# Kernel optimization log

Measured on AMD Instinct MI355X. Metric: run time of the kernel, lower is better.

## Reference

```python
import jax, jax.numpy as jnp
import numpy as np

B, S, D, H, Dh, F = 1, 2048, 2048, 24, 128, 8192  # batch, seq, dim, heads, dim_head, ff hidden
SCALE = Dh ** -0.5


def _layernorm(x, g, b, eps=1e-5):
    mu = jnp.mean(x, axis=-1, keepdims=True)
    var = jnp.var(x, axis=-1, keepdims=True)
    return (x - mu) * jax.lax.rsqrt(var + eps) * g + b


def _rmsnorm(x, g, eps=1e-5):
    ms = jnp.mean(jnp.square(x), axis=-1, keepdims=True)
    return x * jax.lax.rsqrt(ms + eps) * g


def setup_inputs() -> dict:
    key = jax.random.key(0)
    ks = jax.random.split(key, 8)
    w = lambda k, sh: (jax.random.normal(k, sh, jnp.float32) * (1.0 / np.sqrt(sh[0]))).astype(jnp.float32)
    return {
        "x": jax.random.normal(ks[0], (B, S, D), jnp.float32),
        "ln_g": jnp.ones((D,), jnp.float32),
        "ln_b": jnp.zeros((D,), jnp.float32),
        "attn_g": jnp.ones((D,), jnp.float32),  # RingAttention prenorm (RMSNorm) gamma
        "Wq": w(ks[1], (D, H * Dh)),
        "Wk": w(ks[2], (D, H * Dh)),
        "Wv": w(ks[3], (D, H * Dh)),
        "Wo": w(ks[4], (H * Dh, D)),
        "W1": w(ks[5], (D, F)),
        "b1": jnp.zeros((F,), jnp.float32),
        "W2": w(ks[6], (F, D)),
        "b2": jnp.zeros((D,), jnp.float32),
    }


def reference(x, ln_g, ln_b, attn_g, Wq, Wk, Wv, Wo, W1, b1, W2, b2):
    # outer block LayerNorm
    x = _layernorm(x, ln_g, ln_b)

    # --- causal multi-head attention (math-equivalent to ring attention) ---
    h = _rmsnorm(x, attn_g)  # attention's internal prenorm
    q = (h @ Wq).reshape(B, S, H, Dh)
    k = (h @ Wk).reshape(B, S, H, Dh)
    v = (h @ Wv).reshape(B, S, H, Dh)
    scores = jnp.einsum("bqhd,bkhd->bhqk", q, k) * SCALE  # [B,H,S,S]
    causal = jnp.tril(jnp.ones((S, S), bool))
    scores = jnp.where(causal, scores, jnp.finfo(scores.dtype).min)
    attn = jax.nn.softmax(scores, axis=-1)
    o = jnp.einsum("bhqk,bkhd->bqhd", attn, v).reshape(B, S, H * Dh)
    x = o @ Wo + x  # residual

    # --- feedforward + residual ---
    x = jax.nn.gelu(x @ W1 + b1) @ W2 + b2 + x
    return x
```

## Files before the change

### kernel.cpp

```cpp
#include <hip/hip_runtime.h>
#include <hip/hip_bf16.h>

#define Sq 2048
#define Dm 2048
#define HDim 3072
#define QKVDim 9216
#define NH 24
#define DH 128
#define FF 8192
#define ATT_SCALE 0.08838834764831845f

using bf16 = __hip_bfloat16;
typedef __attribute__((ext_vector_type(8))) short bf16x8;
typedef __attribute__((ext_vector_type(4))) float f32x4;
typedef unsigned int u32;
typedef unsigned long long u64;
typedef __attribute__((ext_vector_type(4))) u32 u32x4;

__device__ __forceinline__ void gload_lds16(const void* g, void* l) {
    __builtin_amdgcn_global_load_lds(
        (const __attribute__((address_space(1))) void*)g,
        (__attribute__((address_space(3))) void*)l, 16, 0, 0);
}

__global__ __launch_bounds__(256) void ln_rms_kernel(
    const float* __restrict__ x, const float* __restrict__ g, const float* __restrict__ b,
    const float* __restrict__ ag, float* __restrict__ xnf, bf16* __restrict__ h)
{
    __shared__ float redA[4], redB[4], redC[4];
    int row = blockIdx.x;
    int t = threadIdx.x;
    int lane = t & 63, wid = t >> 6;
    const float* xr = x + (size_t)row * Dm;

    float v[8];
    float sum = 0.f, ssq = 0.f;
#pragma unroll
    for (int i = 0; i < 8; i++) {
        float f = xr[t + 256 * i];
        v[i] = f; sum += f; ssq += f * f;
    }
#pragma unroll
    for (int off = 32; off > 0; off >>= 1) {
        sum += __shfl_down(sum, off);
        ssq += __shfl_down(ssq, off);
    }
    if (lane == 0) { redA[wid] = sum; redB[wid] = ssq; }
    __syncthreads();
    sum = redA[0] + redA[1] + redA[2] + redA[3];
    ssq = redB[0] + redB[1] + redB[2] + redB[3];
    float mu = sum * (1.f / Dm);
    float var = ssq * (1.f / Dm) - mu * mu;
    float rstd = rsqrtf(var + 1e-5f);

    float xn[8];
    float s2 = 0.f;
#pragma unroll
    for (int i = 0; i < 8; i++) {
        int col = t + 256 * i;
        float xv = (v[i] - mu) * rstd * g[col] + b[col];
        xn[i] = xv;
        xnf[(size_t)row * Dm + col] = xv;
        s2 += xv * xv;
    }
#pragma unroll
    for (int off = 32; off > 0; off >>= 1) s2 += __shfl_down(s2, off);
    if (lane == 0) redC[wid] = s2;
    __syncthreads();
    s2 = redC[0] + redC[1] + redC[2] + redC[3];
    float rms = rsqrtf(s2 * (1.f / Dm) + 1e-5f);
#pragma unroll
    for (int i = 0; i < 8; i++) {
        int col = t + 256 * i;
        h[(size_t)row * Dm + col] = __float2bfloat16(xn[i] * rms * ag[col]);
    }
}

__global__ __launch_bounds__(256) void transpose_cvt_kernel(
    const float* __restrict__ W, bf16* __restrict__ Wt, int K, int N)
{
    __shared__ float tile[32][36];
    int n0 = blockIdx.x * 32, k0 = blockIdx.y * 32;
    int t = threadIdx.x;
    int r = t >> 3, c4 = (t & 7) * 4;
    f32x4 v = *reinterpret_cast<const f32x4*>(W + (size_t)(k0 + r) * N + n0 + c4);
    *reinterpret_cast<f32x4*>(&tile[r][c4]) = v;
    __syncthreads();
    int nr = t >> 3, kc = (t & 7) * 4;
    bf16 o4[4];
    o4[0] = __float2bfloat16(tile[kc + 0][nr]);
    o4[1] = __float2bfloat16(tile[kc + 1][nr]);
    o4[2] = __float2bfloat16(tile[kc + 2][nr]);
    o4[3] = __float2bfloat16(tile[kc + 3][nr]);
    *reinterpret_cast<u64*>(Wt + (size_t)(n0 + nr) * K + k0 + kc) = *reinterpret_cast<const u64*>(o4);
}

__global__ __launch_bounds__(256) void transpose_cvt3_kernel(
    const float* __restrict__ Wa, const float* __restrict__ Wb, const float* __restrict__ Wc,
    bf16* __restrict__ Wt, int K, int N)
{
    __shared__ float tile[32][36];
    const float* W = blockIdx.z == 0 ? Wa : (blockIdx.z == 1 ? Wb : Wc);
    bf16* dst = Wt + (size_t)blockIdx.z * N * K;
    int n0 = blockIdx.x * 32, k0 = blockIdx.y * 32;
    int t = threadIdx.x;
    int r = t >> 3, c4 = (t & 7) * 4;
    f32x4 v = *reinterpret_cast<const f32x4*>(W + (size_t)(k0 + r) * N + n0 + c4);
    *reinterpret_cast<f32x4*>(&tile[r][c4]) = v;
    __syncthreads();
    int nr = t >> 3, kc = (t & 7) * 4;
    bf16 o4[4];
    o4[0] = __float2bfloat16(tile[kc + 0][nr]);
    o4[1] = __float2bfloat16(tile[kc + 1][nr]);
    o4[2] = __float2bfloat16(tile[kc + 2][nr]);
    o4[3] = __float2bfloat16(tile[kc + 3][nr]);
    *reinterpret_cast<u64*>(dst + (size_t)(n0 + nr) * K + k0 + kc) = *reinterpret_cast<const u64*>(o4);
}

__global__ __launch_bounds__(256) void cvt_prefill_kernel(
    const float* __restrict__ xnf, const float* __restrict__ bias,
    bf16* __restrict__ hb, float* __restrict__ o, int N)
{
    int i = (blockIdx.x * 256 + threadIdx.x) * 8;
    int col = i % N;
    f32x4 a = *reinterpret_cast<const f32x4*>(xnf + i);
    f32x4 b = *reinterpret_cast<const f32x4*>(xnf + i + 4);
    bf16 r[8];
#pragma unroll
    for (int j = 0; j < 4; j++) { r[j] = __float2bfloat16(a[j]); r[4 + j] = __float2bfloat16(b[j]); }
    *reinterpret_cast<u32x4*>(hb + i) = *reinterpret_cast<const u32x4*>(r);
    f32x4 b0 = *reinterpret_cast<const f32x4*>(bias + col);
    f32x4 b1v = *reinterpret_cast<const f32x4*>(bias + col + 4);
    f32x4 o0 = {a[0] + b0[0], a[1] + b0[1], a[2] + b0[2], a[3] + b0[3]};
    f32x4 o1 = {b[0] + b1v[0], b[1] + b1v[1], b[2] + b1v[2], b[3] + b1v[3]};
    *reinterpret_cast<f32x4*>(o + i) = o0;
    *reinterpret_cast<f32x4*>(o + i + 4) = o1;
}

template <int EPI>
__global__ __launch_bounds__(256, 4) void gemm_kernel(
    const bf16* __restrict__ A, const bf16* __restrict__ Bt,
    int M, int N, int K, int Ksplit,
    bf16* Cb, float* Cf, const float* __restrict__ bias)
{
    __shared__ __align__(16) bf16 As[128 * 64];
    __shared__ __align__(16) bf16 Bs[128 * 64];
    int m0 = blockIdx.y * 128, n0 = blockIdx.x * 128;
    int kbeg = blockIdx.z * Ksplit, kend = kbeg + Ksplit;
    int tid = threadIdx.x;
    int lane = tid & 63, w = tid >> 6;
    int wr = w >> 1, wc = w & 1;
    int l15 = lane & 15, lhi = lane >> 4;

    int srow = lane >> 3;
    int scol = ((lane & 7) ^ (lane >> 3)) * 8;

    const f32x4 zero4 = {0.f, 0.f, 0.f, 0.f};
    f32x4 acc[4][4];
#pragma unroll
    for (int m = 0; m < 4; m++)
#pragma unroll
        for (int n = 0; n < 4; n++) acc[m][n] = zero4;

    for (int k0 = kbeg; k0 < kend; k0 += 64) {
        __syncthreads();
#pragma unroll
        for (int c = 0; c < 4; c++) {
            int row = w * 32 + c * 8 + srow;
            gload_lds16(A + (size_t)(m0 + row) * K + k0 + scol,
                        (char*)As + w * 4096 + c * 1024);
            gload_lds16(Bt + (size_t)(n0 + row) * K + k0 + scol,
                        (char*)Bs + w * 4096 + c * 1024);
        }
        __syncthreads();
#pragma unroll
        for (int ks = 0; ks < 2; ks++) {
            bf16x8 af[4], bfr[4];
#pragma unroll
            for (int m = 0; m < 4; m++) {
                int r = wr * 64 + m * 16 + l15;
                af[m] = *reinterpret_cast<const bf16x8*>(
                    &As[r * 64 + (((ks << 2) + lhi) ^ (r & 7)) * 8]);
            }
#pragma unroll
            for (int n = 0; n < 4; n++) {
                int r = wc * 64 + n * 16 + l15;
                bfr[n] = *reinterpret_cast<const bf16x8*>(
                    &Bs[r * 64 + (((ks << 2) + lhi) ^ (r & 7)) * 8]);
            }
#pragma unroll
            for (int m = 0; m < 4; m++)
#pragma unroll
                for (int n = 0; n < 4; n++)
                    acc[m][n] = __builtin_amdgcn_mfma_f32_16x16x32_bf16(af[m], bfr[n], acc[m][n], 0, 0, 0);
        }
    }

#pragma unroll
    for (int m = 0; m < 4; m++) {
        int row = m0 + wr * 64 + m * 16 + lhi * 4;
#pragma unroll
        for (int n = 0; n < 4; n++) {
            int col = n0 + wc * 64 + n * 16 + l15;
#pragma unroll
            for (int j = 0; j < 4; j++) {
                float vv = acc[m][n][j];
                size_t idx = (size_t)(row + j) * N + col;
                if (EPI == 0) {
                    Cb[idx] = __float2bfloat16(vv);
                } else if (EPI == 2) {
                    float o = vv + bias[col];
                    float u = 1.5957691216057308f * (o + 0.044715f * o * o * o);
                    Cb[idx] = __float2bfloat16(o / (1.0f + __expf(-u)));
                } else {
                    atomicAdd(&Cf[idx], vv);
                }
            }
        }
    }
}

__global__ __launch_bounds__(256) void attn_kernel(
    const bf16* __restrict__ qkv, bf16* __restrict__ o)
{
    __shared__ __align__(16) bf16 KsF[2][64 * 128];
    __shared__ __align__(16) bf16 VtF[2][128 * 72];
    __shared__ __align__(16) bf16 Pl[4][16][76];
    int rank = blockIdx.x;
    int qb = (Sq / 64 - 1) - rank / NH;
    int head = rank % NH;
    const bf16* q = qkv + head * DH;
    const bf16* k = qkv + HDim + head * DH;
    const bf16* v = qkv + 2 * HDim + head * DH;
    int tid = threadIdx.x, lane = tid & 63, w = tid >> 6;
    int l15 = lane & 15, lhi = lane >> 4;
    int qrow0 = qb * 64 + w * 16;

    bf16x8 aq[4];
    const bf16* qbase = q + (size_t)(qrow0 + l15) * QKVDim;
#pragma unroll
    for (int kk = 0; kk < 4; kk++)
        aq[kk] = *reinterpret_cast<const bf16x8*>(qbase + kk * 32 + lhi * 8);

    bf16x8 vones;
#pragma unroll
    for (int j = 0; j < 8; j++) vones[j] = (short)0x3F80;

    int krow_st = w * 16;
    int vkv = lhi * 2 + (w & 1) + (w >> 1) * 8;
    int vd0 = l15 * 8;
    int vxr = l15 & 7;
    const bf16* vbase = v + (size_t)vkv * QKVDim + vd0;

    const f32x4 zero4 = {0.f, 0.f, 0.f, 0.f};
    f32x4 acc_o[8];
#pragma unroll
    for (int db = 0; db < 8; db++) acc_o[db] = zero4;
    f32x4 acc_l = zero4;
    float mrow[4];
#pragma unroll
    for (int r = 0; r < 4; r++) mrow[r] = -1e30f;

    {
#pragma unroll
        for (int c = 0; c < 4; c++) {
            int row = krow_st + c * 4 + lhi;
            int cb = l15 ^ (row & 7);
            gload_lds16(k + (size_t)row * QKVDim + cb * 8,
                        (char*)&KsF[0][0] + w * 4096 + c * 1024);
        }
#pragma unroll
        for (int i = 0; i < 4; i++) {
            int kv = vkv + i * 16;
            bf16x8 vv = *reinterpret_cast<const bf16x8*>(vbase + (size_t)(i * 16) * QKVDim);
            int vb = kv >> 3, kr = kv & 7;
#pragma unroll
            for (int j = 0; j < 8; j++)
                VtF[0][(vd0 + j) * 72 + ((vb ^ vxr) << 3) + kr] = ((const bf16*)&vv)[j];
        }
        __syncthreads();
    }

    for (int kb = 0; kb <= qb; kb++) {
        int kv0 = kb * 64;
        int p = kb & 1;
        bf16x8 vreg[4];
        bool pref = (kb < qb);
        if (pref) {
            int nv0 = kv0 + 64;
#pragma unroll
            for (int c = 0; c < 4; c++) {
                int row = krow_st + c * 4 + lhi;
                int cb = l15 ^ (row & 7);
                gload_lds16(k + (size_t)(nv0 + row) * QKVDim + cb * 8,
                            (char*)&KsF[p ^ 1][0] + w * 4096 + c * 1024);
            }
#pragma unroll
            for (int i = 0; i < 4; i++)
                vreg[i] = *reinterpret_cast<const bf16x8*>(
                    vbase + (size_t)(nv0 + i * 16) * QKVDim);
        }

        f32x4 sacc[4];
#pragma unroll
        for (int nb = 0; nb < 4; nb++) {
            sacc[nb] = zero4;
            int krow = nb * 16 + l15;
#pragma unroll
            for (int kk = 0; kk < 4; kk++) {
                const char* kp = (const char*)&KsF[p][0] + krow * 256 +
                                 ((kk * 64 + lhi * 16) ^ ((krow & 7) << 4));
                bf16x8 bk = *reinterpret_cast<const bf16x8*>(kp);
                sacc[nb] = __builtin_amdgcn_mfma_f32_16x16x32_bf16(aq[kk], bk, sacc[nb], 0, 0, 0);
            }
        }

        bool diag = (kb == qb);
        float sv[4][4];
        float pm[4];
#pragma unroll
        for (int r = 0; r < 4; r++) pm[r] = -1e30f;
#pragma unroll
        for (int nb = 0; nb < 4; nb++) {
            int kvc = kv0 + nb * 16 + l15;
#pragma unroll
            for (int r = 0; r < 4; r++) {
                int qr = qrow0 + lhi * 4 + r;
                float s = sacc[nb][r] * ATT_SCALE;
                if (diag && kvc > qr) s = -1e30f;
                sv[nb][r] = s;
                pm[r] = fmaxf(pm[r], s);
            }
        }
#pragma unroll
        for (int off = 1; off < 16; off <<= 1)
#pragma unroll
            for (int r = 0; r < 4; r++)
                pm[r] = fmaxf(pm[r], __shfl_xor(pm[r], off));

        float nm[4];
        bool need = false;
#pragma unroll
        for (int r = 0; r < 4; r++) {
            nm[r] = fmaxf(mrow[r], pm[r]);
            need = need || (pm[r] > mrow[r] + 8.f);
        }
        if (__any(need)) {
#pragma unroll
            for (int r = 0; r < 4; r++) {
                float sc = __expf(mrow[r] - nm[r]);
                mrow[r] = nm[r];
                acc_l[r] *= sc;
#pragma unroll
                for (int db = 0; db < 8; db++) acc_o[db][r] *= sc;
            }
        }

#pragma unroll
        for (int nb = 0; nb < 4; nb++)
#pragma unroll
            for (int r = 0; r < 4; r++)
                sv[nb][r] = __expf(sv[nb][r] - mrow[r]);

#pragma unroll
        for (int nb = 0; nb < 4; nb++)
#pragma unroll
            for (int r = 0; r < 4; r++)
                Pl[w][lhi * 4 + r][nb * 16 + l15] = __float2bfloat16(sv[nb][r]);

#pragma unroll
        for (int ks = 0; ks < 2; ks++) {
            bf16x8 ap = *reinterpret_cast<const bf16x8*>(&Pl[w][l15][ks * 32 + lhi * 8]);
            acc_l = __builtin_amdgcn_mfma_f32_16x16x32_bf16(ap, vones, acc_l, 0, 0, 0);
#pragma unroll
            for (int db = 0; db < 8; db++) {
                int dv = db * 16 + l15;
                int blk = (ks * 4 + lhi) ^ ((dv >> 3) & 7);
                bf16x8 bv = *reinterpret_cast<const bf16x8*>(&VtF[p][dv * 72 + blk * 8]);
                acc_o[db] = __builtin_amdgcn_mfma_f32_16x16x32_bf16(ap, bv, acc_o[db], 0, 0, 0);
            }
        }

        if (pref) {
#pragma unroll
            for (int i = 0; i < 4; i++) {
                int kv = vkv + i * 16;
                int vb = kv >> 3, kr = kv & 7;
#pragma unroll
                for (int j = 0; j < 8; j++)
                    VtF[p ^ 1][(vd0 + j) * 72 + ((vb ^ vxr) << 3) + kr] = ((const bf16*)&vreg[i])[j];
            }
        }
        __syncthreads();
    }

#pragma unroll
    for (int db = 0; db < 8; db++)
#pragma unroll
        for (int r = 0; r < 4; r++) {
            int qr = qrow0 + lhi * 4 + r;
            float val = acc_o[db][r] / acc_l[r];
            o[(size_t)qr * HDim + head * DH + db * 16 + l15] = __float2bfloat16(val);
        }
}

extern "C" void kernel_launch(void* const* d_in, const int* in_sizes, int n_in,
                              void* d_out, int out_size, void* d_ws, size_t ws_size,
                              hipStream_t stream)
{
    const float* x     = (const float*)d_in[0];
    const float* ln_g  = (const float*)d_in[1];
    const float* ln_b  = (const float*)d_in[2];
    const float* attng = (const float*)d_in[3];
    const float* Wq    = (const float*)d_in[4];
    const float* Wk    = (const float*)d_in[5];
    const float* Wv    = (const float*)d_in[6];
    const float* Wo    = (const float*)d_in[7];
    const float* W1    = (const float*)d_in[8];
    const float* b1    = (const float*)d_in[9];
    const float* W2    = (const float*)d_in[10];
    const float* b2    = (const float*)d_in[11];
    float* out = (float*)d_out;
    char* ws = (char*)d_ws;

    bf16*  wbuf = (bf16*)(ws + 0);
    float* xnf  = (float*)(ws + 39845888);
    bf16*  hbuf = (bf16*)(ws + 56623104);
    bf16*  qkv  = (bf16*)(ws + 65011712);
    bf16*  ob_  = (bf16*)(ws + 102760448);
    bf16*  gb_  = qkv;

    ln_rms_kernel<<<Sq, 256, 0, stream>>>(x, ln_g, ln_b, attng, xnf, hbuf);

    transpose_cvt3_kernel<<<dim3(HDim / 32, Dm / 32, 3), 256, 0, stream>>>(
        Wq, Wk, Wv, wbuf, Dm, HDim);
    gemm_kernel<0><<<dim3(QKVDim / 128, Sq / 128, 1), 256, 0, stream>>>(
        hbuf, wbuf, Sq, QKVDim, Dm, Dm, qkv, nullptr, nullptr);

    attn_kernel<<<dim3(NH * Sq / 64), 256, 0, stream>>>(qkv, ob_);

    transpose_cvt_kernel<<<dim3(Dm / 32, HDim / 32), 256, 0, stream>>>(Wo, wbuf, HDim, Dm);
    gemm_kernel<4><<<dim3(Dm / 128, Sq / 128, 2), 256, 0, stream>>>(
        ob_, wbuf, Sq, Dm, HDim, HDim / 2, nullptr, xnf, nullptr);
    cvt_prefill_kernel<<<(Sq * Dm) / (256 * 8), 256, 0, stream>>>(xnf, b2, hbuf, out, Dm);

    transpose_cvt_kernel<<<dim3(FF / 32, Dm / 32), 256, 0, stream>>>(W1, wbuf, Dm, FF);
    gemm_kernel<2><<<dim3(FF / 128, Sq / 128, 1), 256, 0, stream>>>(
        hbuf, wbuf, Sq, FF, Dm, Dm, gb_, nullptr, b1);

    transpose_cvt_kernel<<<dim3(Dm / 32, FF / 32), 256, 0, stream>>>(W2, wbuf, FF, Dm);
    gemm_kernel<4><<<dim3(Dm / 128, Sq / 128, 2), 256, 0, stream>>>(
        gb_, wbuf, Sq, Dm, FF, FF / 2, nullptr, out, nullptr);
}
```

Before: 461.9 us.

## Add 256x256-tile 8-wave GEMM with interleaved staging for Wo/W1/W2

Adds a new GEMM kernel with 256x256 output tiles, 512 threads, double-buffered LDS filled by direct global-to-LDS loads, and a four-phase schedule that interleaves fragment loads, next-tile staging, and MFMA bursts under raised wave priority. The Wo, W1 and W2 projections now use it, and split-K rises from 2 to 4 for the two atomic-accumulate GEMMs. Larger tiles raise arithmetic intensity and cut global reloads of A and B, while the extra splits keep enough blocks in flight. The cost is more barriers per K step, heavier register pressure from 32 accumulators per lane, and twice as many atomic adds.

Measured after the change: 515.1 us. 11.5% more time.

```diff
diff --git a/kernel.cpp b/kernel.cpp
--- a/kernel.cpp
+++ b/kernel.cpp
@@ -22,6 +22,10 @@
         (const __attribute__((address_space(1))) void*)g,
         (__attribute__((address_space(3))) void*)l, 16, 0, 0);
 }
+
+#define BARRIER() do { asm volatile("" ::: "memory"); \
+    __builtin_amdgcn_s_barrier(); \
+    asm volatile("" ::: "memory"); } while (0)
 
 __global__ __launch_bounds__(256) void ln_rms_kernel(
     const float* __restrict__ x, const float* __restrict__ g, const float* __restrict__ b,
@@ -220,6 +224,156 @@
     }
 }
 
+template <int EPI>
+__global__ __launch_bounds__(512, 2) void gemm256_kernel(
+    const bf16* __restrict__ A, const bf16* __restrict__ Bt,
+    int M, int N, int K, int Ksplit,
+    bf16* Cb, float* Cf, const float* __restrict__ bias)
+{
+    __shared__ __align__(16) bf16 As[2][2][128 * 64];
+    __shared__ __align__(16) bf16 Bs[2][2][128 * 64];
+    int m0 = blockIdx.y * 256, n0 = blockIdx.x * 256;
+    int kbeg = blockIdx.z * Ksplit;
+    int nt = Ksplit >> 6;
+    int tid = threadIdx.x;
+    int lane = tid & 63, w = tid >> 6;
+    int wr = w >> 2, wc = w & 3;
+    int l15 = lane & 15, lhi = lane >> 4;
+    int hb = wc >> 1;
+    int x7 = l15 & 7;
+
+    int lrow = lane >> 3;
+    int scol = ((lane & 7) ^ lrow) * 8;
+
+    f32x4 acc[8][4];
+    const f32x4 zero4 = {0.f, 0.f, 0.f, 0.f};
+#pragma unroll
+    for (int mm = 0; mm < 8; mm++)
+#pragma unroll
+        for (int nn = 0; nn < 4; nn++) acc[mm][nn] = zero4;
+
+    auto stage = [&](int op, int h, int tau) {
+        int ts = tau < nt ? tau : 0;
+        const bf16* base = op ? Bt : A;
+        int r0 = (op ? n0 : m0) + h * 128 + w * 8 + lrow;
+        const bf16* src = base + (size_t)r0 * K + kbeg + ts * 64 + scol;
+        char* dst = (char*)(op ? &Bs[tau & 1][h][0] : &As[tau & 1][h][0]) + w * 1024;
+        gload_lds16(src, dst);
+        gload_lds16(src + (size_t)64 * K, dst + 8192);
+    };
+
+    stage(0, 0, 0); stage(0, 1, 0); stage(1, 0, 0); stage(1, 1, 0);
+    stage(0, 0, 1); stage(0, 1, 1);
+    asm volatile("s_waitcnt vmcnt(4)" ::: "memory");
+    BARRIER();
+
+    for (int t = 0; t < nt; ++t) {
+        int buf = t & 1;
+        bf16x8 a0[4][2], a1[4][2], bA[2][2], bB[2][2];
+
+#pragma unroll
+        for (int m = 0; m < 4; m++) {
+            int r = m * 16 + l15;
+            a0[m][0] = *reinterpret_cast<const bf16x8*>(&As[buf][wr][r * 64 + ((lhi ^ x7) << 3)]);
+            a0[m][1] = *reinterpret_cast<const bf16x8*>(&As[buf][wr][r * 64 + (((4 + lhi) ^ x7) << 3)]);
+        }
+#pragma unroll
+        for (int n = 0; n < 2; n++) {
+            int rb = (wc & 1) * 64 + n * 16 + l15;
+            bA[n][0] = *reinterpret_cast<const bf16x8*>(&Bs[buf][hb][rb * 64 + ((lhi ^ x7) << 3)]);
+            bA[n][1] = *reinterpret_cast<const bf16x8*>(&Bs[buf][hb][rb * 64 + (((4 + lhi) ^ x7) << 3)]);
+        }
+        stage(1, 0, t + 1);
+        BARRIER();
+        __builtin_amdgcn_s_setprio(1);
+#pragma unroll
+        for (int m = 0; m < 4; m++)
+#pragma unroll
+            for (int n = 0; n < 2; n++) {
+                acc[m][n] = __builtin_amdgcn_mfma_f32_16x16x32_bf16(a0[m][0], bA[n][0], acc[m][n], 0, 0, 0);
+                acc[m][n] = __builtin_amdgcn_mfma_f32_16x16x32_bf16(a0[m][1], bA[n][1], acc[m][n], 0, 0, 0);
+            }
+        __builtin_amdgcn_s_setprio(0);
+        BARRIER();
+
+#pragma unroll
+        for (int m = 0; m < 4; m++) {
+            int r = 64 + m * 16 + l15;
+            a1[m][0] = *reinterpret_cast<const bf16x8*>(&As[buf][wr][r * 64 + ((lhi ^ x7) << 3)]);
+            a1[m][1] = *reinterpret_cast<const bf16x8*>(&As[buf][wr][r * 64 + (((4 + lhi) ^ x7) << 3)]);
+        }
+        stage(1, 1, t + 1);
+        BARRIER();
+        __builtin_amdgcn_s_setprio(1);
+#pragma unroll
+        for (int m = 0; m < 4; m++)
+#pragma unroll
+            for (int n = 0; n < 2; n++) {
+                acc[4 + m][n] = __builtin_amdgcn_mfma_f32_16x16x32_bf16(a1[m][0], bA[n][0], acc[4 + m][n], 0, 0, 0);
+                acc[4 + m][n] = __builtin_amdgcn_mfma_f32_16x16x32_bf16(a1[m][1], bA[n][1], acc[4 + m][n], 0, 0, 0);
+            }
+        __builtin_amdgcn_s_setprio(0);
+        BARRIER();
+
+#pragma unroll
+        for (int n = 0; n < 2; n++) {
+            int rb = (wc & 1) * 64 + (2 + n) * 16 + l15;
+            bB[n][0] = *reinterpret_cast<const bf16x8*>(&Bs[buf][hb][rb * 64 + ((lhi ^ x7) << 3)]);
+            bB[n][1] = *reinterpret_cast<const bf16x8*>(&Bs[buf][hb][rb * 64 + (((4 + lhi) ^ x7) << 3)]);
+        }
+        stage(0, 0, t + 2);
+        BARRIER();
+        __builtin_amdgcn_s_setprio(1);
+#pragma unroll
+        for (int m = 0; m < 4; m++)
+#pragma unroll
+            for (int n = 0; n < 2; n++) {
+                acc[m][2 + n] = __builtin_amdgcn_mfma_f32_16x16x32_bf16(a0[m][0], bB[n][0], acc[m][2 + n], 0, 0, 0);
+                acc[m][2 + n] = __builtin_amdgcn_mfma_f32_16x16x32_bf16(a0[m][1], bB[n][1], acc[m][2 + n], 0, 0, 0);
+            }
+        __builtin_amdgcn_s_setprio(0);
+        BARRIER();
+
+        stage(0, 1, t + 2);
+        asm volatile("s_waitcnt vmcnt(4)" ::: "memory");
+        BARRIER();
+        __builtin_amdgcn_s_setprio(1);
+#pragma unroll
+        for (int m = 0; m < 4; m++)
+#pragma unroll
+            for (int n = 0; n < 2; n++) {
+                acc[4 + m][2 + n] = __builtin_amdgcn_mfma_f32_16x16x32_bf16(a1[m][0], bB[n][0], acc[4 + m][2 + n], 0, 0, 0);
+                acc[4 + m][2 + n] = __builtin_amdgcn_mfma_f32_16x16x32_bf16(a1[m][1], bB[n][1], acc[4 + m][2 + n], 0, 0, 0);
+            }
+        __builtin_amdgcn_s_setprio(0);
+        BARRIER();
+    }
+    asm volatile("s_waitcnt vmcnt(0)" ::: "memory");
+
+#pragma unroll
+    for (int mm = 0; mm < 8; mm++) {
+        int row = m0 + wr * 128 + mm * 16 + lhi * 4;
+#pragma unroll
+        for (int nn = 0; nn < 4; nn++) {
+            int col = n0 + wc * 64 + nn * 16 + l15;
+#pragma unroll
+            for (int j = 0; j < 4; j++) {
+                float vv = acc[mm][nn][j];
+                size_t idx = (size_t)(row + j) * N + col;
+                if (EPI == 0) {
+                    Cb[idx] = __float2bfloat16(vv);
+                } else if (EPI == 2) {
+                    float o = vv + bias[col];
+                    float u = 1.5957691216057308f * (o + 0.044715f * o * o * o);
+                    Cb[idx] = __float2bfloat16(o / (1.0f + __expf(-u)));
+                } else {
+                    atomicAdd(&Cf[idx], vv);
+                }
+            }
+        }
+    }
+}
+
 __global__ __launch_bounds__(256) void attn_kernel(
     const bf16* __restrict__ qkv, bf16* __restrict__ o)
 {
@@ -440,15 +594,15 @@
     attn_kernel<<<dim3(NH * Sq / 64), 256, 0, stream>>>(qkv, ob_);
 
     transpose_cvt_kernel<<<dim3(Dm / 32, HDim / 32), 256, 0, stream>>>(Wo, wbuf, HDim, Dm);
-    gemm_kernel<4><<<dim3(Dm / 128, Sq / 128, 2), 256, 0, stream>>>(
-        ob_, wbuf, Sq, Dm, HDim, HDim / 2, nullptr, xnf, nullptr);
+    gemm256_kernel<4><<<dim3(Dm / 256, Sq / 256, 4), 512, 0, stream>>>(
+        ob_, wbuf, Sq, Dm, HDim, HDim / 4, nullptr, xnf, nullptr);
     cvt_prefill_kernel<<<(Sq * Dm) / (256 * 8), 256, 0, stream>>>(xnf, b2, hbuf, out, Dm);
 
     transpose_cvt_kernel<<<dim3(FF / 32, Dm / 32), 256, 0, stream>>>(W1, wbuf, Dm, FF);
-    gemm_kernel<2><<<dim3(FF / 128, Sq / 128, 1), 256, 0, stream>>>(
+    gemm256_kernel<2><<<dim3(FF / 256, Sq / 256, 1), 512, 0, stream>>>(
         hbuf, wbuf, Sq, FF, Dm, Dm, gb_, nullptr, b1);
 
     transpose_cvt_kernel<<<dim3(Dm / 32, FF / 32), 256, 0, stream>>>(W2, wbuf, FF, Dm);
-    gemm_kernel<4><<<dim3(Dm / 128, Sq / 128, 2), 256, 0, stream>>>(
-        gb_, wbuf, Sq, Dm, FF, FF / 2, nullptr, out, nullptr);
-}
+    gemm256_kernel<4><<<dim3(Dm / 256, Sq / 256, 4), 512, 0, stream>>>(
+        gb_, wbuf, Sq, Dm, FF, FF / 4, nullptr, out, nullptr);
+}
```

## Widen attention blocks to 128 query rows with 8 waves sharing K/V tiles

Applied to the files above, without the earlier changes.

The attention kernel now runs 512 threads per block covering 128 query rows, so each K/V tile loaded into shared memory serves twice as many queries. This halves global K/V traffic per query and the number of blocks. V storage drops to a single buffer guarded by an extra barrier, and waves skip score work on fully masked tiles. MFMA sections are wrapped in s_setprio. The cost is an extra __syncthreads per tile, idle waves on diagonal tiles, and fewer blocks for load balancing.

Measured after the change: 454.9 us. No clear change (-1.5%).

```diff
diff --git a/kernel.cpp b/kernel.cpp
--- a/kernel.cpp
+++ b/kernel.cpp
@@ -220,21 +220,21 @@
     }
 }
 
-__global__ __launch_bounds__(256) void attn_kernel(
+__global__ __launch_bounds__(512) void attn_kernel(
     const bf16* __restrict__ qkv, bf16* __restrict__ o)
 {
     __shared__ __align__(16) bf16 KsF[2][64 * 128];
-    __shared__ __align__(16) bf16 VtF[2][128 * 72];
-    __shared__ __align__(16) bf16 Pl[4][16][76];
+    __shared__ __align__(16) bf16 VtF[128 * 72];
+    __shared__ __align__(16) bf16 Pl[8][16][76];
     int rank = blockIdx.x;
-    int qb = (Sq / 64 - 1) - rank / NH;
+    int qb = (Sq / 128 - 1) - rank / NH;
     int head = rank % NH;
     const bf16* q = qkv + head * DH;
     const bf16* k = qkv + HDim + head * DH;
     const bf16* v = qkv + 2 * HDim + head * DH;
     int tid = threadIdx.x, lane = tid & 63, w = tid >> 6;
     int l15 = lane & 15, lhi = lane >> 4;
-    int qrow0 = qb * 64 + w * 16;
+    int qrow0 = qb * 128 + w * 16;
 
     bf16x8 aq[4];
     const bf16* qbase = q + (size_t)(qrow0 + l15) * QKVDim;
@@ -246,7 +246,6 @@
 #pragma unroll
     for (int j = 0; j < 8; j++) vones[j] = (short)0x3F80;
 
-    int krow_st = w * 16;
     int vkv = lhi * 2 + (w & 1) + (w >> 1) * 8;
     int vd0 = l15 * 8;
     int vxr = l15 & 7;
@@ -261,134 +260,144 @@
 #pragma unroll
     for (int r = 0; r < 4; r++) mrow[r] = -1e30f;
 
+    int nt = 2 * qb + 2;
+
     {
 #pragma unroll
-        for (int c = 0; c < 4; c++) {
-            int row = krow_st + c * 4 + lhi;
+        for (int c = 0; c < 2; c++) {
+            int row = w * 8 + c * 4 + lhi;
             int cb = l15 ^ (row & 7);
             gload_lds16(k + (size_t)row * QKVDim + cb * 8,
-                        (char*)&KsF[0][0] + w * 4096 + c * 1024);
-        }
-#pragma unroll
-        for (int i = 0; i < 4; i++) {
-            int kv = vkv + i * 16;
-            bf16x8 vv = *reinterpret_cast<const bf16x8*>(vbase + (size_t)(i * 16) * QKVDim);
+                        (char*)&KsF[0][0] + w * 2048 + c * 1024);
+        }
+#pragma unroll
+        for (int i = 0; i < 2; i++) {
+            int kv = vkv + i * 32;
+            bf16x8 vv = *reinterpret_cast<const bf16x8*>(vbase + (size_t)(i * 32) * QKVDim);
             int vb = kv >> 3, kr = kv & 7;
 #pragma unroll
             for (int j = 0; j < 8; j++)
-                VtF[0][(vd0 + j) * 72 + ((vb ^ vxr) << 3) + kr] = ((const bf16*)&vv)[j];
+                VtF[(vd0 + j) * 72 + ((vb ^ vxr) << 3) + kr] = ((const bf16*)&vv)[j];
         }
         __syncthreads();
     }
 
-    for (int kb = 0; kb <= qb; kb++) {
+    for (int kb = 0; kb < nt; kb++) {
         int kv0 = kb * 64;
         int p = kb & 1;
-        bf16x8 vreg[4];
-        bool pref = (kb < qb);
+        bf16x8 vreg[2];
+        bool pref = (kb + 1 < nt);
         if (pref) {
             int nv0 = kv0 + 64;
 #pragma unroll
-            for (int c = 0; c < 4; c++) {
-                int row = krow_st + c * 4 + lhi;
+            for (int c = 0; c < 2; c++) {
+                int row = w * 8 + c * 4 + lhi;
                 int cb = l15 ^ (row & 7);
                 gload_lds16(k + (size_t)(nv0 + row) * QKVDim + cb * 8,
-                            (char*)&KsF[p ^ 1][0] + w * 4096 + c * 1024);
-            }
-#pragma unroll
-            for (int i = 0; i < 4; i++)
+                            (char*)&KsF[p ^ 1][0] + w * 2048 + c * 1024);
+            }
+#pragma unroll
+            for (int i = 0; i < 2; i++)
                 vreg[i] = *reinterpret_cast<const bf16x8*>(
-                    vbase + (size_t)(nv0 + i * 16) * QKVDim);
-        }
-
-        f32x4 sacc[4];
-#pragma unroll
-        for (int nb = 0; nb < 4; nb++) {
-            sacc[nb] = zero4;
-            int krow = nb * 16 + l15;
-#pragma unroll
-            for (int kk = 0; kk < 4; kk++) {
-                const char* kp = (const char*)&KsF[p][0] + krow * 256 +
-                                 ((kk * 64 + lhi * 16) ^ ((krow & 7) << 4));
-                bf16x8 bk = *reinterpret_cast<const bf16x8*>(kp);
-                sacc[nb] = __builtin_amdgcn_mfma_f32_16x16x32_bf16(aq[kk], bk, sacc[nb], 0, 0, 0);
-            }
-        }
-
-        bool diag = (kb == qb);
-        float sv[4][4];
-        float pm[4];
-#pragma unroll
-        for (int r = 0; r < 4; r++) pm[r] = -1e30f;
-#pragma unroll
-        for (int nb = 0; nb < 4; nb++) {
-            int kvc = kv0 + nb * 16 + l15;
+                    vbase + (size_t)(nv0 + i * 32) * QKVDim);
+        }
+
+        bool active = (kv0 <= qrow0 + 15);
+        if (active) {
+            f32x4 sacc[4];
+            __builtin_amdgcn_s_setprio(1);
+#pragma unroll
+            for (int nb = 0; nb < 4; nb++) {
+                sacc[nb] = zero4;
+                int krow = nb * 16 + l15;
+#pragma unroll
+                for (int kk = 0; kk < 4; kk++) {
+                    const char* kp = (const char*)&KsF[p][0] + krow * 256 +
+                                     ((kk * 64 + lhi * 16) ^ ((krow & 7) << 4));
+                    bf16x8 bk = *reinterpret_cast<const bf16x8*>(kp);
+                    sacc[nb] = __builtin_amdgcn_mfma_f32_16x16x32_bf16(aq[kk], bk, sacc[nb], 0, 0, 0);
+                }
+            }
+            __builtin_amdgcn_s_setprio(0);
+
+            bool msk = (kv0 + 63 > qrow0);
+            float sv[4][4];
+            float pm[4];
+#pragma unroll
+            for (int r = 0; r < 4; r++) pm[r] = -1e30f;
+#pragma unroll
+            for (int nb = 0; nb < 4; nb++) {
+                int kvc = kv0 + nb * 16 + l15;
+#pragma unroll
+                for (int r = 0; r < 4; r++) {
+                    int qr = qrow0 + lhi * 4 + r;
+                    float s = sacc[nb][r] * ATT_SCALE;
+                    if (msk && kvc > qr) s = -1e30f;
+                    sv[nb][r] = s;
+                    pm[r] = fmaxf(pm[r], s);
+                }
+            }
+#pragma unroll
+            for (int off = 1; off < 16; off <<= 1)
+#pragma unroll
+                for (int r = 0; r < 4; r++)
+                    pm[r] = fmaxf(pm[r], __shfl_xor(pm[r], off));
+
+            float nm[4];
+            bool need = false;
 #pragma unroll
             for (int r = 0; r < 4; r++) {
-                int qr = qrow0 + lhi * 4 + r;
-                float s = sacc[nb][r] * ATT_SCALE;
-                if (diag && kvc > qr) s = -1e30f;
-                sv[nb][r] = s;
-                pm[r] = fmaxf(pm[r], s);
-            }
-        }
-#pragma unroll
-        for (int off = 1; off < 16; off <<= 1)
-#pragma unroll
-            for (int r = 0; r < 4; r++)
-                pm[r] = fmaxf(pm[r], __shfl_xor(pm[r], off));
-
-        float nm[4];
-        bool need = false;
-#pragma unroll
-        for (int r = 0; r < 4; r++) {
-            nm[r] = fmaxf(mrow[r], pm[r]);
-            need = need || (pm[r] > mrow[r] + 8.f);
-        }
-        if (__any(need)) {
-#pragma unroll
-            for (int r = 0; r < 4; r++) {
-                float sc = __expf(mrow[r] - nm[r]);
-                mrow[r] = nm[r];
-                acc_l[r] *= sc;
-#pragma unroll
-                for (int db = 0; db < 8; db++) acc_o[db][r] *= sc;
-            }
-        }
-
-#pragma unroll
-        for (int nb = 0; nb < 4; nb++)
-#pragma unroll
-            for (int r = 0; r < 4; r++)
-                sv[nb][r] = __expf(sv[nb][r] - mrow[r]);
-
-#pragma unroll
-        for (int nb = 0; nb < 4; nb++)
-#pragma unroll
-            for (int r = 0; r < 4; r++)
-                Pl[w][lhi * 4 + r][nb * 16 + l15] = __float2bfloat16(sv[nb][r]);
-
-#pragma unroll
-        for (int ks = 0; ks < 2; ks++) {
-            bf16x8 ap = *reinterpret_cast<const bf16x8*>(&Pl[w][l15][ks * 32 + lhi * 8]);
-            acc_l = __builtin_amdgcn_mfma_f32_16x16x32_bf16(ap, vones, acc_l, 0, 0, 0);
-#pragma unroll
-            for (int db = 0; db < 8; db++) {
-                int dv = db * 16 + l15;
-                int blk = (ks * 4 + lhi) ^ ((dv >> 3) & 7);
-                bf16x8 bv = *reinterpret_cast<const bf16x8*>(&VtF[p][dv * 72 + blk * 8]);
-                acc_o[db] = __builtin_amdgcn_mfma_f32_16x16x32_bf16(ap, bv, acc_o[db], 0, 0, 0);
-            }
-        }
-
+                nm[r] = fmaxf(mrow[r], pm[r]);
+                need = need || (pm[r] > mrow[r] + 8.f);
+            }
+            if (__any(need)) {
+#pragma unroll
+                for (int r = 0; r < 4; r++) {
+                    float sc = __expf(mrow[r] - nm[r]);
+                    mrow[r] = nm[r];
+                    acc_l[r] *= sc;
+#pragma unroll
+                    for (int db = 0; db < 8; db++) acc_o[db][r] *= sc;
+                }
+            }
+
+#pragma unroll
+            for (int nb = 0; nb < 4; nb++)
+#pragma unroll
+                for (int r = 0; r < 4; r++)
+                    sv[nb][r] = __expf(sv[nb][r] - mrow[r]);
+
+#pragma unroll
+            for (int nb = 0; nb < 4; nb++)
+#pragma unroll
+                for (int r = 0; r < 4; r++)
+                    Pl[w][lhi * 4 + r][nb * 16 + l15] = __float2bfloat16(sv[nb][r]);
+
+            __builtin_amdgcn_s_setprio(1);
+#pragma unroll
+            for (int ks = 0; ks < 2; ks++) {
+                bf16x8 ap = *reinterpret_cast<const bf16x8*>(&Pl[w][l15][ks * 32 + lhi * 8]);
+                acc_l = __builtin_amdgcn_mfma_f32_16x16x32_bf16(ap, vones, acc_l, 0, 0, 0);
+#pragma unroll
+                for (int db = 0; db < 8; db++) {
+                    int dv = db * 16 + l15;
+                    int blk = (ks * 4 + lhi) ^ ((dv >> 3) & 7);
+                    bf16x8 bv = *reinterpret_cast<const bf16x8*>(&VtF[dv * 72 + blk * 8]);
+                    acc_o[db] = __builtin_amdgcn_mfma_f32_16x16x32_bf16(ap, bv, acc_o[db], 0, 0, 0);
+                }
+            }
+            __builtin_amdgcn_s_setprio(0);
+        }
+
+        __syncthreads();
         if (pref) {
 #pragma unroll
-            for (int i = 0; i < 4; i++) {
-                int kv = vkv + i * 16;
+            for (int i = 0; i < 2; i++) {
+                int kv = vkv + i * 32;
                 int vb = kv >> 3, kr = kv & 7;
 #pragma unroll
                 for (int j = 0; j < 8; j++)
-                    VtF[p ^ 1][(vd0 + j) * 72 + ((vb ^ vxr) << 3) + kr] = ((const bf16*)&vreg[i])[j];
+                    VtF[(vd0 + j) * 72 + ((vb ^ vxr) << 3) + kr] = ((const bf16*)&vreg[i])[j];
             }
         }
         __syncthreads();
@@ -437,7 +446,7 @@
     gemm_kernel<0><<<dim3(QKVDim / 128, Sq / 128, 1), 256, 0, stream>>>(
         hbuf, wbuf, Sq, QKVDim, Dm, Dm, qkv, nullptr, nullptr);
 
-    attn_kernel<<<dim3(NH * Sq / 64), 256, 0, stream>>>(qkv, ob_);
+    attn_kernel<<<dim3(NH * Sq / 128), 512, 0, stream>>>(qkv, ob_);
 
     transpose_cvt_kernel<<<dim3(Dm / 32, HDim / 32), 256, 0, stream>>>(Wo, wbuf, HDim, Dm);
     gemm_kernel<4><<<dim3(Dm / 128, Sq / 128, 2), 256, 0, stream>>>(
```
